# Performance work log

Hardware: AMD Instinct MI355X
Metric: run time of the kernel (lower is better)

The kernel has to match this reference:

```python
import jax, jax.numpy as jnp
import numpy as np
from jax import lax

B, S, D, H = 4, 1024, 1024, 16
DK = D // H


def setup_inputs() -> dict:
    key = jax.random.key(0)
    ks = jax.random.split(key, 8)
    s = 0.02
    return {
        "text_embeddings": jax.random.normal(ks[0], (B, S, D), jnp.float32),
        "text_mask": jnp.ones((B, S), jnp.int32),
        "W_G": jax.random.normal(ks[1], (D, D), jnp.float32) * s,
        "b_G": jnp.zeros((D,), jnp.float32),
        "Wq": jax.random.normal(ks[2], (D, D), jnp.float32) * s,
        "bq": jnp.zeros((D,), jnp.float32),
        "Wk": jax.random.normal(ks[3], (D, D), jnp.float32) * s,
        "bk": jnp.zeros((D,), jnp.float32),
        "conv_w": jax.random.normal(ks[4], (D, H, 3), jnp.float32) * s,
        "conv_b": jnp.zeros((D,), jnp.float32),
    }


def _rope_tables(seq_len, dk):
    # interleaved sinusoidal tables, each value repeated twice along feature dim
    pos = jnp.arange(seq_len, dtype=jnp.float32)[:, None]            # [S,1]
    inv = jnp.power(10000.0, -2.0 * jnp.arange(dk // 2, dtype=jnp.float32) / dk)
    ang = pos * inv                                                   # [S,DK/2]
    cos_pos = jnp.repeat(jnp.cos(ang), 2, axis=-1)[None, None]        # [1,1,S,DK]
    sin_pos = jnp.repeat(jnp.sin(ang), 2, axis=-1)[None, None]
    return cos_pos, sin_pos


def reference(text_embeddings, text_mask, W_G, b_G, Wq, bq, Wk, bk, conv_w, conv_b):
    b, s, d = text_embeddings.shape
    g = text_embeddings @ W_G + b_G                                   # [B,S,D]
    q = (g @ Wq + bq).reshape(b, s, H, DK).transpose(0, 2, 1, 3)      # [B,H,S,DK]
    k = (g @ Wk + bk).reshape(b, s, H, DK).transpose(0, 2, 1, 3)

    cos_pos, sin_pos = _rope_tables(s, DK)
    # NOTE: query rotation uses +q_odd (module does NOT negate for q), key uses -k_odd
    qw2 = jnp.stack([q[..., 1::2], q[..., ::2]], axis=-1).reshape(q.shape)
    qw = q * cos_pos + qw2 * sin_pos
    kw2 = jnp.stack([-k[..., 1::2], k[..., ::2]], axis=-1).reshape(k.shape)
    kw = k * cos_pos + kw2 * sin_pos

    scores = jnp.einsum("bhqd,bhkd->bhqk", qw, kw) / np.float32(np.sqrt(DK))
    mask = text_mask[:, None, None, :]                                # [B,1,1,S]
    scores = jnp.where(mask == 0, jnp.float32(-1e9), scores)
    p_attn = jax.nn.softmax(scores, axis=-1)                          # [B,H,S,S]

    row0 = p_attn[:, :, 0, :]                                         # [B,H,S]
    conv = lax.conv_general_dilated(
        row0, conv_w, window_strides=(1,), padding=[(1, 1)],
        dimension_numbers=("NCH", "OIH", "NCH"))                      # [B,D,S]
    return jax.nn.relu(conv + conv_b[None, :, None])
```

## Files before the change

kernel.cpp:

```cpp
#include <hip/hip_runtime.h>
#include <math.h>

#define B_  4
#define S_  1024
#define D_  1024
#define H_  16

typedef __bf16 bf16x8 __attribute__((ext_vector_type(8)));
typedef float  f32x4  __attribute__((ext_vector_type(4)));

__device__ __forceinline__ unsigned short f2bf(float f) {
  unsigned u = __builtin_bit_cast(unsigned, f);
  u = (u + 0x7FFFu + ((u >> 16) & 1u)) >> 16;
  return (unsigned short)u;
}
__device__ __forceinline__ float bf2f(unsigned short h) {
  unsigned u = ((unsigned)h) << 16;
  return __builtin_bit_cast(float, u);
}

__device__ __forceinline__ void gl_lds16(const void* g, void* lds) {
  __builtin_amdgcn_global_load_lds(
      (const __attribute__((address_space(1))) unsigned int*)(unsigned long long)g,
      (__attribute__((address_space(3))) unsigned int*)(unsigned int)(unsigned long long)lds,
      16, 0, 0);
}

__global__ __launch_bounds__(256) void prep_kernel(
    const float* __restrict__ X, const float* __restrict__ W_G,
    const float* __restrict__ Wk, const float* __restrict__ bG,
    unsigned short* __restrict__ WGbf, unsigned short* __restrict__ WkT,
    float* __restrict__ partG, float* __restrict__ partB) {
  __shared__ float tle[32][33];
  __shared__ float gs2[4][32];
  __shared__ float bgs[32];
  const int blk = blockIdx.x;
  const int tid = threadIdx.x;

  if (blk < 512) {
    const int i = (blk * 256 + tid) * 2;
    const float4 v0 = ((const float4*)W_G)[i];
    const float4 v1 = ((const float4*)W_G)[i + 1];
    ushort4 h0, h1;
    h0.x = f2bf(v0.x); h0.y = f2bf(v0.y); h0.z = f2bf(v0.z); h0.w = f2bf(v0.w);
    h1.x = f2bf(v1.x); h1.y = f2bf(v1.y); h1.z = f2bf(v1.z); h1.w = f2bf(v1.w);
    ((ushort4*)WGbf)[i] = h0;
    ((ushort4*)WGbf)[i + 1] = h1;
  } else if (blk < 1536) {
    const int t = blk - 512;
    const int k0 = (t & 31) * 32;
    const int n0 = (t >> 5) * 32;
    const int tx = tid & 31;
    const int ty = tid >> 5;
#pragma unroll
    for (int r = 0; r < 32; r += 8)
      tle[ty + r][tx] = Wk[(size_t)(k0 + ty + r) * 1024 + n0 + tx];
    __syncthreads();
#pragma unroll
    for (int r = 0; r < 32; r += 8)
      WkT[(size_t)(n0 + ty + r) * 1024 + k0 + tx] = f2bf(tle[tx][ty + r]);
  } else if (blk < 1664) {
    const int bl = blk - 1536;
    const int sg = bl >> 2;
    const int mg = bl & 3;
    if (tid < 128) {
      const int b = tid >> 5, kk = tid & 31;
      gs2[b][kk] = X[(size_t)b * S_ * D_ + sg * 32 + kk];
    }
    __syncthreads();
    const int mid = mg * 256 + tid;
    float a0 = 0.f, a1 = 0.f, a2 = 0.f, a3 = 0.f;
#pragma unroll
    for (int kk = 0; kk < 32; ++kk) {
      const float w = W_G[(size_t)(sg * 32 + kk) * 1024 + mid];
      a0 = fmaf(gs2[0][kk], w, a0);
      a1 = fmaf(gs2[1][kk], w, a1);
      a2 = fmaf(gs2[2][kk], w, a2);
      a3 = fmaf(gs2[3][kk], w, a3);
    }
    partG[(size_t)(sg * 4 + 0) * 1024 + mid] = a0;
    partG[(size_t)(sg * 4 + 1) * 1024 + mid] = a1;
    partG[(size_t)(sg * 4 + 2) * 1024 + mid] = a2;
    partG[(size_t)(sg * 4 + 3) * 1024 + mid] = a3;
  } else {
    const int bl = blk - 1664;
    const int sl = bl >> 2;
    const int ng = bl & 3;
    if (tid < 32) bgs[tid] = bG[sl * 32 + tid];
    __syncthreads();
    const int n = ng * 256 + tid;
    float a = 0.f;
#pragma unroll
    for (int kk = 0; kk < 32; ++kk)
      a = fmaf(bgs[kk], Wk[(size_t)(sl * 32 + kk) * 1024 + n], a);
    partB[(size_t)sl * 1024 + n] = a;
  }
}

#define GM 64
#define GN 128

__global__ __launch_bounds__(256) void gemm_bf16(
    const unsigned short* __restrict__ A, const unsigned short* __restrict__ BT,
    const float* __restrict__ bias, unsigned short* __restrict__ C,
    const int mShift, const int nGemmBlocks,
    const float* __restrict__ Wq, float* __restrict__ part,
    const float* __restrict__ partG, const float* __restrict__ bG,
    const float* __restrict__ partB, const float* __restrict__ bk,
    float* __restrict__ biasK,
    const float* __restrict__ X, unsigned short* __restrict__ Xbf,
    float* __restrict__ tab,
    const float* __restrict__ bq, const int* __restrict__ mask,
    float* __restrict__ scores, float* __restrict__ mS) {
  __shared__ __align__(16) unsigned short As[3][2][GM * 32];
  __shared__ __align__(16) unsigned short Bs[3][2][GN * 32];
  __shared__ float gs[4][32];
  __shared__ float q0s[128];
  __shared__ float sc[64][9];

  const int flat = blockIdx.x;
  const int tid  = threadIdx.x;

  if (flat >= nGemmBlocks) {
    const int eb = flat - nGemmBlocks;
    if (eb < 128) {
      const int slab = eb >> 2;
      const int n = (eb & 3) * 256 + tid;
      if (tid < 128) {
        const int b = tid >> 5, kk = tid & 31;
        float v = bG[slab * 32 + kk];
        const float* pg = partG + (size_t)b * 1024 + slab * 32 + kk;
#pragma unroll
        for (int sg = 0; sg < 32; ++sg) v += pg[(size_t)sg * 4096];
        gs[b][kk] = v;
      }
      __syncthreads();
      float a0 = 0.f, a1 = 0.f, a2 = 0.f, a3 = 0.f;
#pragma unroll
      for (int kk = 0; kk < 32; ++kk) {
        const float w = Wq[(size_t)(slab * 32 + kk) * D_ + n];
        a0 = fmaf(gs[0][kk], w, a0);
        a1 = fmaf(gs[1][kk], w, a1);
        a2 = fmaf(gs[2][kk], w, a2);
        a3 = fmaf(gs[3][kk], w, a3);
      }
      part[(size_t)(slab * 4 + 0) * D_ + n] = a0;
      part[(size_t)(slab * 4 + 1) * D_ + n] = a1;
      part[(size_t)(slab * 4 + 2) * D_ + n] = a2;
      part[(size_t)(slab * 4 + 3) * D_ + n] = a3;
    } else if (eb < 132) {
      const int n = (eb - 128) * 256 + tid;
      float v = bk[n];
#pragma unroll
      for (int sl = 0; sl < 32; ++sl) v += partB[(size_t)sl * 1024 + n];
      biasK[n] = v;
    } else if (eb < 260) {
      const int idx = (eb - 132) * 256 + tid;
      const int s = idx >> 5, j = idx & 31;
      const float inv = (float)exp(-(double)j * (9.210340371976182736 / 32.0));
      float sn, c;
      sincosf((float)s * inv, &sn, &c);
      tab[(size_t)s * 64 + 2 * j] = c;
      tab[(size_t)s * 64 + 2 * j + 1] = sn;
    } else {
      const int i = ((eb - 260) * 256 + tid) * 2;
      const float4 v0 = ((const float4*)X)[i];
      const float4 v1 = ((const float4*)X)[i + 1];
      ushort4 h0, h1;
      h0.x = f2bf(v0.x); h0.y = f2bf(v0.y); h0.z = f2bf(v0.z); h0.w = f2bf(v0.w);
      h1.x = f2bf(v1.x); h1.y = f2bf(v1.y); h1.z = f2bf(v1.z); h1.w = f2bf(v1.w);
      ((ushort4*)Xbf)[i] = h0;
      ((ushort4*)Xbf)[i + 1] = h1;
    }
    return;
  }

  const int bx = flat >> mShift;
  const int by = flat & ((1 << mShift) - 1);
  const int wv   = tid >> 6;
  const int lane = tid & 63;
  const int m0 = by * GM;
  const int n0 = bx * GN;

  if (scores && tid < 128) {
    const int nq = n0 + tid;
    float v = bq[nq];
#pragma unroll
    for (int sl2 = 0; sl2 < 32; ++sl2)
      v += part[(size_t)(sl2 * 4 + (m0 >> 10)) * D_ + nq];
    q0s[tid] = v;
  }

  const int colOff = (lane & 3) * 8;
  const size_t aOff  = (size_t)(m0 + 16 * wv + (lane >> 2)) * 1024 + colOff;
  const size_t bOff0 = (size_t)(n0 + 32 * wv + (lane >> 2)) * 1024 + colOff;
  const size_t bOff1 = bOff0 + (size_t)16 * 1024;

  const int l15  = lane & 15;
  const int quad = lane >> 4;

  f32x4 acc[4][2];
#pragma unroll
  for (int i = 0; i < 4; ++i)
#pragma unroll
    for (int j = 0; j < 2; ++j) acc[i][j] = (f32x4){0.f, 0.f, 0.f, 0.f};

  auto STG = [&](int bufi, int kk) {
#pragma unroll
    for (int ks = 0; ks < 2; ++ks) {
      gl_lds16(A  + aOff  + kk + ks * 32, &As[bufi][ks][wv * 512]);
      gl_lds16(BT + bOff0 + kk + ks * 32, &Bs[bufi][ks][wv * 1024]);
      gl_lds16(BT + bOff1 + kk + ks * 32, &Bs[bufi][ks][wv * 1024 + 512]);
    }
  };

  STG(0, 0);
  STG(1, 64);

#pragma unroll 1
  for (int t = 0; t < 16; ++t) {
    const int cur = t - (t / 3) * 3;
    if (t < 14) {
      const int nb = (t + 2) - ((t + 2) / 3) * 3;
      STG(nb, (t + 2) * 64);
      asm volatile("s_waitcnt vmcnt(12)" ::: "memory");
    } else if (t == 14) {
      asm volatile("s_waitcnt vmcnt(6)" ::: "memory");
    } else {
      asm volatile("s_waitcnt vmcnt(0)" ::: "memory");
    }
    __builtin_amdgcn_s_barrier();
    __builtin_amdgcn_sched_barrier(0);

#pragma unroll
    for (int ks = 0; ks < 2; ++ks) {
      bf16x8 af[4], bfr[2];
#pragma unroll
      for (int mi = 0; mi < 4; ++mi)
        af[mi] = *(const bf16x8*)(&As[cur][ks][(mi * 16 + l15) * 32 + quad * 8]);
#pragma unroll
      for (int ni = 0; ni < 2; ++ni)
        bfr[ni] = *(const bf16x8*)(
            &Bs[cur][ks][(wv * 32 + ni * 16 + l15) * 32 + quad * 8]);
#pragma unroll
      for (int mi = 0; mi < 4; ++mi)
#pragma unroll
        for (int ni = 0; ni < 2; ++ni)
          acc[mi][ni] = __builtin_amdgcn_mfma_f32_16x16x32_bf16(
              af[mi], bfr[ni], acc[mi][ni], 0, 0, 0);
    }
    __builtin_amdgcn_sched_barrier(0);
    __builtin_amdgcn_s_barrier();
  }

  if (scores) {
    const int b_i   = m0 >> 10;
    const int sbase = m0 & 1023;
#pragma unroll
    for (int ni = 0; ni < 2; ++ni) {
      const int n_loc = wv * 32 + ni * 16 + l15;
      const float bv  = bias[n0 + n_loc];
      const float q0a = q0s[n_loc];
      const float q0b = q0s[n_loc ^ 1];
      const float sq  = (n_loc & 1) ? -q0b : q0b;
      const int j2    = (n_loc & 63) & ~1;
#pragma unroll
      for (int mi = 0; mi < 4; ++mi) {
#pragma unroll
        for (int r = 0; r < 4; ++r) {
          const int s_loc = mi * 16 + quad * 4 + r;
          const float2 cs =
              *(const float2*)(tab + (size_t)(sbase + s_loc) * 64 + j2);
          const float coef = q0a * cs.x + sq * cs.y;
          float v = (acc[mi][ni][r] + bv) * coef;
          v += __shfl_xor(v, 1);
          v += __shfl_xor(v, 2);
          v += __shfl_xor(v, 4);
          v += __shfl_xor(v, 8);
          if (l15 == 0) sc[s_loc][wv * 2 + ni] = v;
        }
      }
    }
    __syncthreads();
    if (tid < 128) {
      const int h_loc = tid >> 6;
      const int s_loc = tid & 63;
      const float* row = sc[s_loc];
      float dot = (row[h_loc * 4 + 0] + row[h_loc * 4 + 1]) +
                  (row[h_loc * 4 + 2] + row[h_loc * 4 + 3]);
      dot *= 0.125f;
      const int s = sbase + s_loc;
      if (mask[b_i * S_ + s] == 0) dot = -1e9f;
      const int bh = b_i * H_ + (bx * 2 + h_loc);
      scores[(size_t)bh * S_ + s] = dot;
      float mx = dot;
#pragma unroll
      for (int off = 16; off >= 1; off >>= 1)
        mx = fmaxf(mx, __shfl_xor(mx, off, 32));
      float e = expf(dot - mx);
#pragma unroll
      for (int off = 16; off >= 1; off >>= 1) e += __shfl_xor(e, off, 32);
      if ((s_loc & 31) == 0) {
        const int ch = ((by & 15) << 1) + (s_loc >> 5);
        mS[((size_t)bh * 32 + ch) * 2 + 0] = mx;
        mS[((size_t)bh * 32 + ch) * 2 + 1] = e;
      }
    }
    return;
  }

#pragma unroll
  for (int ni = 0; ni < 2; ++ni) {
    const int n = n0 + wv * 32 + ni * 16 + l15;
    const float bv = bias ? bias[n] : 0.f;
#pragma unroll
    for (int mi = 0; mi < 4; ++mi) {
#pragma unroll
      for (int r = 0; r < 4; ++r) {
        const int m = m0 + mi * 16 + quad * 4 + r;
        C[(size_t)m * 1024 + n] = f2bf(acc[mi][ni][r] + bv);
      }
    }
  }
}

__global__ __launch_bounds__(256) void conv_norm_relu_kernel(
    const float* __restrict__ scores, const float* __restrict__ mS,
    const float* __restrict__ cw, const float* __restrict__ cb,
    float* __restrict__ out) {
  const int b  = blockIdx.y;
  const int s0 = blockIdx.x * 64;
  const int o0 = blockIdx.z * 64;
  const int tid = threadIdx.x;
  const int tx = tid & 7;
  const int ty = tid >> 3;

  __shared__ float msh[16], ish[16];
  __shared__ __align__(16) float wT[48][68];
  __shared__ float cbs[64];
  __shared__ __align__(16) float pm[16][104];

  if (tid < 128) {
    const int h = tid >> 3, seg = tid & 7;
    const int bh = b * H_ + h;
    const float* base = mS + (size_t)bh * 64 + seg * 8;
    float m = -3e38f;
#pragma unroll
    for (int q = 0; q < 4; ++q) m = fmaxf(m, base[q * 2]);
    m = fmaxf(m, __shfl_xor(m, 1));
    m = fmaxf(m, __shfl_xor(m, 2));
    m = fmaxf(m, __shfl_xor(m, 4));
    float S = 0.f;
#pragma unroll
    for (int q = 0; q < 4; ++q) S += base[q * 2 + 1] * expf(base[q * 2] - m);
    S += __shfl_xor(S, 1);
    S += __shfl_xor(S, 2);
    S += __shfl_xor(S, 4);
    if (seg == 0) {
      msh[h] = m;
      ish[h] = 1.f / S;
    }
  }
  for (int i = tid; i < 64 * 48; i += 256) {
    const int ol = i / 48, ct = i % 48;
    wT[ct][ol] = cw[(size_t)(o0 + ol) * 48 + ct];
  }
  if (tid < 64) cbs[tid] = cb[o0 + tid];
  __syncthreads();

  for (int i = tid; i < 16 * 66; i += 256) {
    const int c = i / 66, col = i % 66;
    const int gs = s0 - 1 + col;
    pm[c][12 * (col >> 3) + (col & 7)] =
        (gs >= 0 && gs < S_)
            ? expf(scores[(size_t)(b * H_ + c) * S_ + gs] - msh[c]) * ish[c]
            : 0.f;
  }
  __syncthreads();

  float acc[2][8];
#pragma unroll
  for (int i = 0; i < 2; ++i) {
    const float cv = cbs[ty * 2 + i];
#pragma unroll
    for (int j = 0; j < 8; ++j) acc[i][j] = cv;
  }

#pragma unroll
  for (int c = 0; c < 16; ++c) {
    float pl[10];
    const float* base = &pm[c][12 * tx];
    *(float4*)(pl + 0) = *(const float4*)(base + 0);
    *(float4*)(pl + 4) = *(const float4*)(base + 4);
    *(float2*)(pl + 8) = *(const float2*)(&pm[c][12 * (tx + 1)]);
#pragma unroll
    for (int t = 0; t < 3; ++t) {
      float w[2];
      *(float2*)w = *(const float2*)&wT[c * 3 + t][ty * 2];
#pragma unroll
      for (int i = 0; i < 2; ++i)
#pragma unroll
        for (int j = 0; j < 8; ++j)
          acc[i][j] = fmaf(pl[j + t], w[i], acc[i][j]);
    }
  }

#pragma unroll
  for (int i = 0; i < 2; ++i) {
    float* orow =
        out + ((size_t)b * D_ + o0 + ty * 2 + i) * S_ + s0 + tx * 8;
    float4 v0, v1;
    v0.x = fmaxf(acc[i][0], 0.f); v0.y = fmaxf(acc[i][1], 0.f);
    v0.z = fmaxf(acc[i][2], 0.f); v0.w = fmaxf(acc[i][3], 0.f);
    v1.x = fmaxf(acc[i][4], 0.f); v1.y = fmaxf(acc[i][5], 0.f);
    v1.z = fmaxf(acc[i][6], 0.f); v1.w = fmaxf(acc[i][7], 0.f);
    *(float4*)(orow + 0) = v0;
    *(float4*)(orow + 4) = v1;
  }
}

extern "C" void kernel_launch(void* const* d_in, const int* in_sizes, int n_in,
                              void* d_out, int out_size, void* d_ws,
                              size_t ws_size, hipStream_t stream) {
  const float* x    = (const float*)d_in[0];
  const int*   mask = (const int*)d_in[1];
  const float* W_G  = (const float*)d_in[2];
  const float* b_G  = (const float*)d_in[3];
  const float* Wq   = (const float*)d_in[4];
  const float* bq   = (const float*)d_in[5];
  const float* Wk   = (const float*)d_in[6];
  const float* bk   = (const float*)d_in[7];
  const float* cw   = (const float*)d_in[8];
  const float* cb   = (const float*)d_in[9];
  float* out = (float*)d_out;

  char* ws = (char*)d_ws;
  unsigned short* Xbf  = (unsigned short*)(ws);
  unsigned short* WkT  = (unsigned short*)(ws + (16u << 20));
  unsigned short* WGbf = (unsigned short*)(ws + (18u << 20));
  unsigned short* WfT  = (unsigned short*)(ws + (20u << 20));
  float* part   = (float*)(ws + (22u << 20));
  float* partG  = (float*)(ws + (22u << 20) + (512u << 10));
  float* partB  = (float*)(ws + (23u << 20));
  float* biasK  = (float*)(ws + (23u << 20) + (128u << 10));
  float* ropeT  = (float*)(ws + (23u << 20) + (256u << 10));
  float* scores = (float*)(ws + (23u << 20) + (512u << 10));
  float* mS     = (float*)(ws + (23u << 20) + (768u << 10));

  prep_kernel<<<1792, 256, 0, stream>>>(x, W_G, Wk, b_G, WGbf, WkT,
                                        partG, partB);
  gemm_bf16<<<2436, 256, 0, stream>>>(WkT, WGbf, nullptr, WfT, 4, 128,
                                      Wq, part, partG, b_G, partB, bk, biasK,
                                      x, Xbf, ropeT,
                                      nullptr, nullptr, nullptr, nullptr);
  gemm_bf16<<<512, 256, 0, stream>>>(Xbf, WfT, biasK, nullptr, 6, 512,
                                     nullptr, part, nullptr, nullptr,
                                     nullptr, nullptr, nullptr,
                                     nullptr, nullptr, ropeT,
                                     bq, mask, scores, mS);
  conv_norm_relu_kernel<<<dim3(16, B_, 16), 256, 0, stream>>>(
      scores, mS, cw, cb, out);
}
```

Measured before the change: 137.2 us.

## Enlarge GEMM tile to 128x128 with 2x2 wave layout and double buffering

Grows the bf16 GEMM block tile from 64x128 to 128x128. Each wave now computes a 64x64 sub-tile in a 2x2 arrangement, which raises MFMA work per LDS fragment load. To keep LDS usage in check, the staging pipeline drops from triple to double buffering with a one-stage-ahead prefetch. The grid sizes, the mShift values and the scores/softmax epilogue indexing are adjusted to match. This halves the GEMM block count, which reduces parallelism on a large-CU GPU, and the shallower prefetch may expose more memory latency.

```diff
diff --git a/kernel.cpp b/kernel.cpp
--- a/kernel.cpp
+++ b/kernel.cpp
@@ -97,7 +97,7 @@
   }
 }
 
-#define GM 64
+#define GM 128
 #define GN 128
 
 __global__ __launch_bounds__(256) void gemm_bf16(
@@ -112,11 +112,11 @@
     float* __restrict__ tab,
     const float* __restrict__ bq, const int* __restrict__ mask,
     float* __restrict__ scores, float* __restrict__ mS) {
-  __shared__ __align__(16) unsigned short As[3][2][GM * 32];
-  __shared__ __align__(16) unsigned short Bs[3][2][GN * 32];
+  __shared__ __align__(16) unsigned short As[2][2][GM * 32];
+  __shared__ __align__(16) unsigned short Bs[2][2][GN * 32];
   __shared__ float gs[4][32];
   __shared__ float q0s[128];
-  __shared__ float sc[64][9];
+  __shared__ float sc[128][9];
 
   const int flat = blockIdx.x;
   const int tid  = threadIdx.x;
@@ -179,6 +179,8 @@
   const int by = flat & ((1 << mShift) - 1);
   const int wv   = tid >> 6;
   const int lane = tid & 63;
+  const int wr   = wv >> 1;
+  const int wc   = wv & 1;
   const int m0 = by * GM;
   const int n0 = bx * GN;
 
@@ -192,40 +194,38 @@
   }
 
   const int colOff = (lane & 3) * 8;
-  const size_t aOff  = (size_t)(m0 + 16 * wv + (lane >> 2)) * 1024 + colOff;
+  const size_t aOff0 = (size_t)(m0 + 32 * wv + (lane >> 2)) * 1024 + colOff;
+  const size_t aOff1 = aOff0 + (size_t)16 * 1024;
   const size_t bOff0 = (size_t)(n0 + 32 * wv + (lane >> 2)) * 1024 + colOff;
   const size_t bOff1 = bOff0 + (size_t)16 * 1024;
 
   const int l15  = lane & 15;
   const int quad = lane >> 4;
 
-  f32x4 acc[4][2];
+  f32x4 acc[4][4];
 #pragma unroll
   for (int i = 0; i < 4; ++i)
 #pragma unroll
-    for (int j = 0; j < 2; ++j) acc[i][j] = (f32x4){0.f, 0.f, 0.f, 0.f};
+    for (int j = 0; j < 4; ++j) acc[i][j] = (f32x4){0.f, 0.f, 0.f, 0.f};
 
   auto STG = [&](int bufi, int kk) {
 #pragma unroll
     for (int ks = 0; ks < 2; ++ks) {
-      gl_lds16(A  + aOff  + kk + ks * 32, &As[bufi][ks][wv * 512]);
+      gl_lds16(A  + aOff0 + kk + ks * 32, &As[bufi][ks][wv * 1024]);
+      gl_lds16(A  + aOff1 + kk + ks * 32, &As[bufi][ks][wv * 1024 + 512]);
       gl_lds16(BT + bOff0 + kk + ks * 32, &Bs[bufi][ks][wv * 1024]);
       gl_lds16(BT + bOff1 + kk + ks * 32, &Bs[bufi][ks][wv * 1024 + 512]);
     }
   };
 
   STG(0, 0);
-  STG(1, 64);
 
 #pragma unroll 1
   for (int t = 0; t < 16; ++t) {
-    const int cur = t - (t / 3) * 3;
-    if (t < 14) {
-      const int nb = (t + 2) - ((t + 2) / 3) * 3;
-      STG(nb, (t + 2) * 64);
-      asm volatile("s_waitcnt vmcnt(12)" ::: "memory");
-    } else if (t == 14) {
-      asm volatile("s_waitcnt vmcnt(6)" ::: "memory");
+    const int cur = t & 1;
+    if (t < 15) {
+      STG(cur ^ 1, (t + 1) * 64);
+      asm volatile("s_waitcnt vmcnt(8)" ::: "memory");
     } else {
       asm volatile("s_waitcnt vmcnt(0)" ::: "memory");
     }
@@ -234,18 +234,19 @@
 
 #pragma unroll
     for (int ks = 0; ks < 2; ++ks) {
-      bf16x8 af[4], bfr[2];
+      bf16x8 af[4], bfr[4];
 #pragma unroll
       for (int mi = 0; mi < 4; ++mi)
-        af[mi] = *(const bf16x8*)(&As[cur][ks][(mi * 16 + l15) * 32 + quad * 8]);
-#pragma unroll
-      for (int ni = 0; ni < 2; ++ni)
+        af[mi] = *(const bf16x8*)(
+            &As[cur][ks][(wr * 64 + mi * 16 + l15) * 32 + quad * 8]);
+#pragma unroll
+      for (int ni = 0; ni < 4; ++ni)
         bfr[ni] = *(const bf16x8*)(
-            &Bs[cur][ks][(wv * 32 + ni * 16 + l15) * 32 + quad * 8]);
+            &Bs[cur][ks][(wc * 64 + ni * 16 + l15) * 32 + quad * 8]);
 #pragma unroll
       for (int mi = 0; mi < 4; ++mi)
 #pragma unroll
-        for (int ni = 0; ni < 2; ++ni)
+        for (int ni = 0; ni < 4; ++ni)
           acc[mi][ni] = __builtin_amdgcn_mfma_f32_16x16x32_bf16(
               af[mi], bfr[ni], acc[mi][ni], 0, 0, 0);
     }
@@ -257,8 +258,8 @@
     const int b_i   = m0 >> 10;
     const int sbase = m0 & 1023;
 #pragma unroll
-    for (int ni = 0; ni < 2; ++ni) {
-      const int n_loc = wv * 32 + ni * 16 + l15;
+    for (int ni = 0; ni < 4; ++ni) {
+      const int n_loc = wc * 64 + ni * 16 + l15;
       const float bv  = bias[n0 + n_loc];
       const float q0a = q0s[n_loc];
       const float q0b = q0s[n_loc ^ 1];
@@ -268,7 +269,7 @@
       for (int mi = 0; mi < 4; ++mi) {
 #pragma unroll
         for (int r = 0; r < 4; ++r) {
-          const int s_loc = mi * 16 + quad * 4 + r;
+          const int s_loc = wr * 64 + mi * 16 + quad * 4 + r;
           const float2 cs =
               *(const float2*)(tab + (size_t)(sbase + s_loc) * 64 + j2);
           const float coef = q0a * cs.x + sq * cs.y;
@@ -277,14 +278,14 @@
           v += __shfl_xor(v, 2);
           v += __shfl_xor(v, 4);
           v += __shfl_xor(v, 8);
-          if (l15 == 0) sc[s_loc][wv * 2 + ni] = v;
+          if (l15 == 0) sc[s_loc][wc * 4 + ni] = v;
         }
       }
     }
     __syncthreads();
-    if (tid < 128) {
-      const int h_loc = tid >> 6;
-      const int s_loc = tid & 63;
+    {
+      const int h_loc = tid >> 7;
+      const int s_loc = tid & 127;
       const float* row = sc[s_loc];
       float dot = (row[h_loc * 4 + 0] + row[h_loc * 4 + 1]) +
                   (row[h_loc * 4 + 2] + row[h_loc * 4 + 3]);
@@ -301,7 +302,7 @@
 #pragma unroll
       for (int off = 16; off >= 1; off >>= 1) e += __shfl_xor(e, off, 32);
       if ((s_loc & 31) == 0) {
-        const int ch = ((by & 15) << 1) + (s_loc >> 5);
+        const int ch = ((by & 7) << 2) + (s_loc >> 5);
         mS[((size_t)bh * 32 + ch) * 2 + 0] = mx;
         mS[((size_t)bh * 32 + ch) * 2 + 1] = e;
       }
@@ -310,14 +311,14 @@
   }
 
 #pragma unroll
-  for (int ni = 0; ni < 2; ++ni) {
-    const int n = n0 + wv * 32 + ni * 16 + l15;
+  for (int ni = 0; ni < 4; ++ni) {
+    const int n = n0 + wc * 64 + ni * 16 + l15;
     const float bv = bias ? bias[n] : 0.f;
 #pragma unroll
     for (int mi = 0; mi < 4; ++mi) {
 #pragma unroll
       for (int r = 0; r < 4; ++r) {
-        const int m = m0 + mi * 16 + quad * 4 + r;
+        const int m = m0 + wr * 64 + mi * 16 + quad * 4 + r;
         C[(size_t)m * 1024 + n] = f2bf(acc[mi][ni][r] + bv);
       }
     }
@@ -449,11 +450,11 @@
 
   prep_kernel<<<1792, 256, 0, stream>>>(x, W_G, Wk, b_G, WGbf, WkT,
                                         partG, partB);
-  gemm_bf16<<<2436, 256, 0, stream>>>(WkT, WGbf, nullptr, WfT, 4, 128,
+  gemm_bf16<<<2372, 256, 0, stream>>>(WkT, WGbf, nullptr, WfT, 3, 64,
                                       Wq, part, partG, b_G, partB, bk, biasK,
                                       x, Xbf, ropeT,
                                       nullptr, nullptr, nullptr, nullptr);
-  gemm_bf16<<<512, 256, 0, stream>>>(Xbf, WfT, biasK, nullptr, 6, 512,
+  gemm_bf16<<<256, 256, 0, stream>>>(Xbf, WfT, biasK, nullptr, 5, 256,
                                      nullptr, part, nullptr, nullptr,
                                      nullptr, nullptr, nullptr,
                                      nullptr, nullptr, ropeT,
```

After: 152.0 us. 1.11x slower.
